# Optimization experiments

Hardware: AMD Instinct MI355X
Metric: run time of the kernel (lower is better)

The kernel has to match this reference:

```python
import jax, jax.numpy as jnp
import numpy as np

B, S, D, H = 4, 2048, 256, 4
DH = D // H
MAX_LEN = 2048


def setup_inputs() -> dict:
    key = jax.random.key(0)
    ks = jax.random.split(key, 12)
    std = 0.02
    inp = {
        "x": jax.random.normal(ks[0], (B, S, D), dtype=jnp.float32),
        "Wq": jax.random.normal(ks[1], (D, D), dtype=jnp.float32) * std,
        "bq": jnp.zeros((D,), dtype=jnp.float32),
        "Wk": jax.random.normal(ks[2], (D, D), dtype=jnp.float32) * std,
        "bk": jnp.zeros((D,), dtype=jnp.float32),
        "Wv": jax.random.normal(ks[3], (D, D), dtype=jnp.float32) * std,
        "bv": jnp.zeros((D,), dtype=jnp.float32),
        "Wo": jax.random.normal(ks[4], (D, D), dtype=jnp.float32) * std,
        "bo": jnp.zeros((D,), dtype=jnp.float32),
        "rel_bias": jax.random.normal(ks[5], (2 * MAX_LEN - 1, H), dtype=jnp.float32) * std,
        "scale": jnp.ones((1,), dtype=jnp.float32) * np.sqrt(DH).astype(np.float32),
        "mask": jnp.ones((B, S), dtype=jnp.int32),
    }
    return inp


def reference(x, Wq, bq, Wk, bk, Wv, bv, Wo, bo, rel_bias, scale, mask):
    b, s, d = x.shape
    # projections (torch Linear: x @ W.T + b), split heads -> (B, H, S, Dh)
    def proj(W, bias):
        return (x @ W.T + bias).reshape(b, s, H, DH).transpose(0, 2, 1, 3)
    Q, K, V = proj(Wq, bq), proj(Wk, bk), proj(Wv, bv)

    # raw (un-softmaxed) scores: (B, H, S, S)
    scores = jnp.einsum("bhqd,bhkd->bhqk", Q, K) / scale[0]

    # relative-position bias gather: idx[i,j] = j - i + s - 1
    seq = jnp.arange(s)
    rel_idx = seq[None, :] - seq[:, None] + s - 1        # (S, S)
    rbias = rel_bias[rel_idx]                            # (S, S, H)
    scores = scores + rbias.transpose(2, 0, 1)[None]     # (1, H, S, S)

    # pairwise padding mask: mask_ij = mask_i * mask_j
    m2 = (mask[:, None, :, None] * mask[:, None, None, :])  # (B, 1, S, S)
    scores = jnp.where(m2 == 0, -jnp.inf, scores)

    # no softmax: plain weighted sum with V
    out = jnp.einsum("bhqk,bhkd->bhqd", scores, V)
    out = out.transpose(0, 2, 1, 3).reshape(b, s, d)
    return out @ Wo.T + bo
```

## Files before the change

kernel.cpp:

```cpp
#include <hip/hip_runtime.h>

#define BB 4
#define SS 2048
#define DD 256
#define HH 4
#define DHH 64
#define NDT 63

typedef unsigned short u16;
typedef __attribute__((ext_vector_type(8))) short bf16x8;
typedef __attribute__((ext_vector_type(4))) float f32x4;

#define MFMA(a, b, c) __builtin_amdgcn_mfma_f32_16x16x32_bf16((a), (b), (c), 0, 0, 0)


__device__ __forceinline__ u16 f2b(float x) {
    union { float f; unsigned u; } v; v.f = x;
    unsigned r = (v.u + 0x7FFFu + ((v.u >> 16) & 1u)) >> 16;
    return (u16)r;
}

__global__ __launch_bounds__(256) void cast_x(
    const float* __restrict__ x, u16* __restrict__ Xkb)
{
    const int th = blockIdx.x * 256 + threadIdx.x;
    const int t = th >> 5;
    const int F0 = (th & 31) * 8;
    float4 a = *(const float4*)(x + (size_t)t * DD + F0);
    float4 b = *(const float4*)(x + (size_t)t * DD + F0 + 4);
    u16 v[8] = { f2b(a.x), f2b(a.y), f2b(a.z), f2b(a.w),
                 f2b(b.x), f2b(b.y), f2b(b.z), f2b(b.w) };
    *(uint4*)(Xkb + (size_t)(F0 >> 5) * 262144 + (size_t)t * 32 + (F0 & 31)) = *(uint4*)v;
}

__global__ __launch_bounds__(256) void cast_w(
    const float* __restrict__ Wq, const float* __restrict__ Wk,
    const float* __restrict__ Wv, const float* __restrict__ Wo,
    u16* __restrict__ Wkb)
{
    const float* src = (blockIdx.y == 0) ? Wq : (blockIdx.y == 1) ? Wk
                     : (blockIdx.y == 2) ? Wv : Wo;
    const int th = blockIdx.x * 256 + threadIdx.x;
    const int o = th >> 5;
    const int k0 = (th & 31) * 8;
    float4 a = *(const float4*)(src + (size_t)o * DD + k0);
    float4 b = *(const float4*)(src + (size_t)o * DD + k0 + 4);
    u16 v[8] = { f2b(a.x), f2b(a.y), f2b(a.z), f2b(a.w),
                 f2b(b.x), f2b(b.y), f2b(b.z), f2b(b.w) };
    *(uint4*)(Wkb + (size_t)blockIdx.y * 65536 + (size_t)(k0 >> 5) * 8192
              + (size_t)o * 32 + (k0 & 31)) = *(uint4*)v;
}

__global__ __launch_bounds__(256) void zero_M(float* __restrict__ Mt)
{
    const int i = blockIdx.x * 256 + threadIdx.x;
    if (i < BB * HH * DHH * DHH) Mt[i] = 0.f;
}

__global__ __launch_bounds__(256) void rtiles_kernel(
    const float* __restrict__ rel_bias, u16* __restrict__ Rtb)
{
    const int h  = blockIdx.x / NDT;
    const int dt = blockIdx.x % NDT;
    const int tid = threadIdx.x;
    const int qq = tid >> 2;
    const int kf0 = (tid & 3) * 16;
    const int base = (dt - 31) * 64 - qq + (SS - 1);

    u16 v[16];
    #pragma unroll
    for (int m = 0; m < 16; ++m)
        v[m] = f2b(rel_bias[(size_t)(base + kf0 + m) * HH + h]);

    u16* dst = Rtb + ((size_t)(h * NDT + dt) * 2 + (kf0 >> 5)) * 2048
             + qq * 32 + (kf0 & 31);
    *(uint4*)dst       = *(uint4*)&v[0];
    *(uint4*)(dst + 8) = *(uint4*)&v[8];
}

__global__ __launch_bounds__(256) void proj_mfma(
    const u16* __restrict__ Xkb, const u16* __restrict__ Wkb,
    const float* __restrict__ bq, const float* __restrict__ bk,
    const float* __restrict__ bv,
    u16* __restrict__ Qkb, u16* __restrict__ Kkb, u16* __restrict__ Vkb)
{
    const int z = blockIdx.z;
    const u16* W = Wkb + (size_t)z * 65536;
    const float* bias = (z == 0) ? bq : (z == 1) ? bk : bv;

    const int tid = threadIdx.x;
    const int w = tid >> 6;
    const int lane = tid & 63;
    const int l15 = lane & 15;
    const int g = lane >> 4;

    const int n0 = blockIdx.x * 64;
    const int o0 = blockIdx.y * 128;

    f32x4 acc[4][2] = {};

    if (z == 0) {
        const int tw = w & 1, ow = w >> 1;
        #pragma unroll
        for (int kb = 0; kb < 8; ++kb) {
            bf16x8 bfrag[2], afrag[4];
            #pragma unroll
            for (int j = 0; j < 2; ++j)
                bfrag[j] = *(const bf16x8*)(Xkb + (size_t)kb * 262144
                          + (size_t)(n0 + tw * 32 + j * 16 + l15) * 32 + g * 8);
            #pragma unroll
            for (int f = 0; f < 4; ++f)
                afrag[f] = *(const bf16x8*)(W + (size_t)kb * 8192
                          + (size_t)(o0 + ow * 64 + f * 16 + l15) * 32 + g * 8);
            #pragma unroll
            for (int f = 0; f < 4; ++f)
                #pragma unroll
                for (int j = 0; j < 2; ++j)
                    acc[f][j] = MFMA(afrag[f], bfrag[j], acc[f][j]);
        }
        #pragma unroll
        for (int f = 0; f < 4; ++f) {
            const int F = o0 + ow * 64 + f * 16 + g * 4;
            float4 bv4 = *(const float4*)(bias + F);
            #pragma unroll
            for (int j = 0; j < 2; ++j) {
                const int t = n0 + tw * 32 + j * 16 + l15;
                const int b = t >> 11, q = t & 2047;
                ushort4 st = { f2b(acc[f][j].x + bv4.x), f2b(acc[f][j].y + bv4.y),
                               f2b(acc[f][j].z + bv4.z), f2b(acc[f][j].w + bv4.w) };
                *(ushort4*)(Qkb + (size_t)b * 524288 + (size_t)(F >> 5) * 65536
                            + (size_t)q * 32 + (F & 31)) = st;
            }
        }
    } else {
        #pragma unroll
        for (int kb = 0; kb < 8; ++kb) {
            bf16x8 bfrag[2], afrag[4];
            #pragma unroll
            for (int j = 0; j < 2; ++j)
                bfrag[j] = *(const bf16x8*)(W + (size_t)kb * 8192
                          + (size_t)(o0 + w * 32 + j * 16 + l15) * 32 + g * 8);
            #pragma unroll
            for (int f = 0; f < 4; ++f)
                afrag[f] = *(const bf16x8*)(Xkb + (size_t)kb * 262144
                          + (size_t)(n0 + f * 16 + l15) * 32 + g * 8);
            #pragma unroll
            for (int f = 0; f < 4; ++f)
                #pragma unroll
                for (int j = 0; j < 2; ++j)
                    acc[f][j] = MFMA(afrag[f], bfrag[j], acc[f][j]);
        }
        u16* T = (z == 1) ? Kkb : Vkb;
        const int b = n0 >> 11;
        const int tloc = n0 & 2047;
        #pragma unroll
        for (int j = 0; j < 2; ++j) {
            const int o = o0 + w * 32 + j * 16 + l15;
            const int h = o >> 6, d = o & 63;
            const float bb = bias[o];
            u16* dst0 = T + (size_t)(b * HH + h) * 131072 + (size_t)d * 32;
            #pragma unroll
            for (int f = 0; f < 4; ++f) {
                const int kblk = (tloc >> 5) + (f >> 1);
                const int off = (f & 1) * 16 + g * 4;
                ushort4 st = { f2b(acc[f][j].x + bb), f2b(acc[f][j].y + bb),
                               f2b(acc[f][j].z + bb), f2b(acc[f][j].w + bb) };
                *(ushort4*)(dst0 + (size_t)kblk * 2048 + off) = st;
            }
        }
    }
}

__global__ __launch_bounds__(256) void calc_M_mfma(
    const u16* __restrict__ Kkb, const u16* __restrict__ Vkb,
    const float* __restrict__ scale, float* __restrict__ Mt)
{
    const int bh = blockIdx.x;
    const int kb0 = blockIdx.y * 8;

    const int tid = threadIdx.x;
    const int w = tid >> 6;
    const int lane = tid & 63;
    const int l15 = lane & 15;
    const int g = lane >> 4;

    const u16* Vb = Vkb + (size_t)bh * 131072;
    const u16* Kb = Kkb + (size_t)bh * 131072;

    f32x4 acc[4] = {};
    #pragma unroll
    for (int kk = 0; kk < 8; ++kk) {
        const size_t kb = kb0 + kk;
        bf16x8 bfrag = *(const bf16x8*)(Kb + kb * 2048 + (size_t)(w * 16 + l15) * 32 + g * 8);
        #pragma unroll
        for (int f = 0; f < 4; ++f) {
            bf16x8 afrag = *(const bf16x8*)(Vb + kb * 2048 + (size_t)(f * 16 + l15) * 32 + g * 8);
            acc[f] = MFMA(afrag, bfrag, acc[f]);
        }
    }

    const float inv_scale = 1.0f / scale[0];
    float* Mg = Mt + (size_t)bh * 4096;
    const int e = w * 16 + l15;
    #pragma unroll
    for (int f = 0; f < 4; ++f) {
        const float* a = (const float*)&acc[f];
        #pragma unroll
        for (int i = 0; i < 4; ++i)
            atomicAdd(Mg + (f * 16 + g * 4 + i) * DHH + e, a[i] * inv_scale);
    }
}

__global__ __launch_bounds__(256) void cvt_M(
    const float* __restrict__ Mt, u16* __restrict__ Mkb)
{
    const int bh = blockIdx.x;
    const int tid = threadIdx.x;
    const int d = tid >> 2;
    const int c = (tid & 3) * 16;
    const float* src = Mt + (size_t)bh * 4096 + d * 64 + c;
    u16 v[16];
    #pragma unroll
    for (int m = 0; m < 16; ++m) v[m] = f2b(src[m]);
    u16* dst = Mkb + (size_t)bh * 4096 + (size_t)(c >> 5) * 2048 + d * 32 + (c & 31);
    *(uint4*)dst       = *(uint4*)&v[0];
    *(uint4*)(dst + 8) = *(uint4*)&v[8];
}

__global__ __launch_bounds__(256) void attn_mfma(
    const u16* __restrict__ Qkb, const u16* __restrict__ Vkb,
    const u16* __restrict__ Mkb, const u16* __restrict__ Rtb,
    u16* __restrict__ attnkb)
{
    const int bh = blockIdx.x;
    const int b = bh >> 2, h = bh & 3;
    const int qs = blockIdx.y;

    const int tid = threadIdx.x;
    const int w = tid >> 6;
    const int lane = tid & 63;
    const int l15 = lane & 15;
    const int g = lane >> 4;

    const int qt = qs * 2 + (w >> 1);
    const int qq0 = (w & 1) * 32;

    const u16* vb = Vkb + (size_t)bh * 131072 + (size_t)l15 * 32 + g * 8;
    const u16* rb = Rtb + (size_t)h * NDT * 4096 + (size_t)(qq0 + l15) * 32 + g * 8;

    f32x4 acc[4][2] = {};
    bf16x8 A0[4], B0[2], A1[4], B1[2];

#define LOAD_IT(it_, A_, B_) do {                                           \
        const int it__ = (it_);                                             \
        const u16* vp = vb + (size_t)it__ * 2048;                           \
        _Pragma("unroll")                                                   \
        for (int f = 0; f < 4; ++f) A_[f] = *(const bf16x8*)(vp + f * 512); \
        const int dt__ = (it__ >> 1) - qt + 31;                             \
        const u16* rp = rb + (size_t)(dt__ * 2 + (it__ & 1)) * 2048;        \
        _Pragma("unroll")                                                   \
        for (int j = 0; j < 2; ++j) B_[j] = *(const bf16x8*)(rp + j * 512); \
    } while (0)

#define MFMA_IT(A_, B_) do {                                                \
        _Pragma("unroll")                                                   \
        for (int f = 0; f < 4; ++f)                                         \
            _Pragma("unroll")                                               \
            for (int j = 0; j < 2; ++j)                                     \
                acc[f][j] = MFMA(A_[f], B_[j], acc[f][j]);                  \
    } while (0)

    LOAD_IT(0, A0, B0);
    LOAD_IT(1, A1, B1);
    for (int it = 0; it < 64; it += 2) {
        MFMA_IT(A0, B0);
        LOAD_IT((it + 2) & 63, A0, B0);
        MFMA_IT(A1, B1);
        LOAD_IT((it + 3) & 63, A1, B1);
    }
#undef LOAD_IT
#undef MFMA_IT

    const int q0w = qs * 128 + w * 32;
    #pragma unroll
    for (int s2 = 0; s2 < 2; ++s2) {
        bf16x8 bfrag[2], afrag[4];
        #pragma unroll
        for (int j = 0; j < 2; ++j)
            bfrag[j] = *(const bf16x8*)(Qkb + (size_t)b * 524288
                      + (size_t)(h * 2 + s2) * 65536
                      + (size_t)(q0w + j * 16 + l15) * 32 + g * 8);
        #pragma unroll
        for (int f = 0; f < 4; ++f)
            afrag[f] = *(const bf16x8*)(Mkb + (size_t)bh * 4096 + (size_t)s2 * 2048
                      + (size_t)(f * 16 + l15) * 32 + g * 8);
        #pragma unroll
        for (int f = 0; f < 4; ++f)
            #pragma unroll
            for (int j = 0; j < 2; ++j)
                acc[f][j] = MFMA(afrag[f], bfrag[j], acc[f][j]);
    }

    #pragma unroll
    for (int f = 0; f < 4; ++f) {
        const int Fb = h * 2 + (f >> 1);
        const int off = (f & 1) * 16 + g * 4;
        #pragma unroll
        for (int j = 0; j < 2; ++j) {
            const int q = q0w + j * 16 + l15;
            ushort4 st = { f2b(acc[f][j].x), f2b(acc[f][j].y),
                           f2b(acc[f][j].z), f2b(acc[f][j].w) };
            *(ushort4*)(attnkb + (size_t)b * 524288 + (size_t)Fb * 65536
                        + (size_t)q * 32 + off) = st;
        }
    }
}

__global__ __launch_bounds__(256) void gemm_out_mfma(
    const u16* __restrict__ attnkb, const u16* __restrict__ Wokb,
    const float* __restrict__ bo, float* __restrict__ out)
{
    const int tid = threadIdx.x;
    const int w = tid >> 6;
    const int lane = tid & 63;
    const int l15 = lane & 15;
    const int g = lane >> 4;

    const int n0 = blockIdx.x * 64;
    const int o0 = blockIdx.y * 128;
    const int tw = w & 1, ow = w >> 1;

    f32x4 acc[4][2] = {};
    #pragma unroll
    for (int kb = 0; kb < 8; ++kb) {
        bf16x8 bfrag[2], afrag[4];
        #pragma unroll
        for (int j = 0; j < 2; ++j) {
            const int t = n0 + tw * 32 + j * 16 + l15;
            const int b = t >> 11, q = t & 2047;
            bfrag[j] = *(const bf16x8*)(attnkb + (size_t)b * 524288
                      + (size_t)kb * 65536 + (size_t)q * 32 + g * 8);
        }
        #pragma unroll
        for (int f = 0; f < 4; ++f)
            afrag[f] = *(const bf16x8*)(Wokb + (size_t)kb * 8192
                      + (size_t)(o0 + ow * 64 + f * 16 + l15) * 32 + g * 8);
        #pragma unroll
        for (int f = 0; f < 4; ++f)
            #pragma unroll
            for (int j = 0; j < 2; ++j)
                acc[f][j] = MFMA(afrag[f], bfrag[j], acc[f][j]);
    }

    #pragma unroll
    for (int f = 0; f < 4; ++f) {
        const int o = o0 + ow * 64 + f * 16 + g * 4;
        float4 bv4 = *(const float4*)(bo + o);
        #pragma unroll
        for (int j = 0; j < 2; ++j) {
            const int t = n0 + tw * 32 + j * 16 + l15;
            float4 st = { acc[f][j].x + bv4.x, acc[f][j].y + bv4.y,
                          acc[f][j].z + bv4.z, acc[f][j].w + bv4.w };
            *(float4*)(out + (size_t)t * DD + o) = st;
        }
    }
}

extern "C" void kernel_launch(void* const* d_in, const int* in_sizes, int n_in,
                              void* d_out, int out_size, void* d_ws, size_t ws_size,
                              hipStream_t stream)
{
    const float* x        = (const float*)d_in[0];
    const float* Wq       = (const float*)d_in[1];
    const float* bq       = (const float*)d_in[2];
    const float* Wk       = (const float*)d_in[3];
    const float* bk       = (const float*)d_in[4];
    const float* Wv       = (const float*)d_in[5];
    const float* bv       = (const float*)d_in[6];
    const float* Wo       = (const float*)d_in[7];
    const float* bo       = (const float*)d_in[8];
    const float* rel_bias = (const float*)d_in[9];
    const float* scale    = (const float*)d_in[10];

    float* out = (float*)d_out;

    const size_t NP = (size_t)BB * SS * DD;
    float* Mt    = (float*)d_ws;
    u16*   Xkb   = (u16*)(Mt + 65536);
    u16*   Wkb   = Xkb + NP;
    u16*   Qkb   = Wkb + 4 * 65536;
    u16*   Kkb   = Qkb + NP;
    u16*   Vkb   = Kkb + NP;
    u16*   attnk = Vkb + NP;
    u16*   Rtb   = attnk + NP;
    u16*   Mkb   = Rtb + (size_t)HH * NDT * 4096;

    cast_x<<<dim3(1024), dim3(256), 0, stream>>>(x, Xkb);
    cast_w<<<dim3(32, 4), dim3(256), 0, stream>>>(Wq, Wk, Wv, Wo, Wkb);
    zero_M<<<dim3(256), dim3(256), 0, stream>>>(Mt);
    rtiles_kernel<<<dim3(HH * NDT), dim3(256), 0, stream>>>(rel_bias, Rtb);

    proj_mfma<<<dim3(128, 2, 3), dim3(256), 0, stream>>>(
        Xkb, Wkb, bq, bk, bv, Qkb, Kkb, Vkb);

    calc_M_mfma<<<dim3(BB * HH, 8), dim3(256), 0, stream>>>(Kkb, Vkb, scale, Mt);
    cvt_M<<<dim3(BB * HH), dim3(256), 0, stream>>>(Mt, Mkb);

    attn_mfma<<<dim3(BB * HH, 16), dim3(256), 0, stream>>>(
        Qkb, Vkb, Mkb, Rtb, attnk);

    gemm_out_mfma<<<dim3(128, 2), dim3(256), 0, stream>>>(
        attnk, Wkb + 3 * 65536, bo, out);
}
```

Measured before the change: 144.6 us.

## Merge prep kernels, split attention over key halves, drop M atomics

Fuses the four preprocessing kernels into one launch. The atomic accumulation of M is replaced by per-split partial buffers, which the attention kernel sums and converts on the fly, so the zero and convert kernels go away. The attention kernel now gives each wave a 64-query tile and splits the key dimension into two halves across blockIdx.z, writing two partial outputs. The output GEMM then reads and sums both. This cuts launch count and atomics and improves MFMA reuse per fragment, at the cost of an extra intermediate buffer and doubled reads in the output GEMM.

```diff
diff --git a/kernel.cpp b/kernel.cpp
--- a/kernel.cpp
+++ b/kernel.cpp
@@ -20,62 +20,53 @@
     return (u16)r;
 }
 
-__global__ __launch_bounds__(256) void cast_x(
-    const float* __restrict__ x, u16* __restrict__ Xkb)
-{
-    const int th = blockIdx.x * 256 + threadIdx.x;
-    const int t = th >> 5;
-    const int F0 = (th & 31) * 8;
-    float4 a = *(const float4*)(x + (size_t)t * DD + F0);
-    float4 b = *(const float4*)(x + (size_t)t * DD + F0 + 4);
-    u16 v[8] = { f2b(a.x), f2b(a.y), f2b(a.z), f2b(a.w),
-                 f2b(b.x), f2b(b.y), f2b(b.z), f2b(b.w) };
-    *(uint4*)(Xkb + (size_t)(F0 >> 5) * 262144 + (size_t)t * 32 + (F0 & 31)) = *(uint4*)v;
-}
-
-__global__ __launch_bounds__(256) void cast_w(
+__global__ __launch_bounds__(256) void prep(
+    const float* __restrict__ x,
     const float* __restrict__ Wq, const float* __restrict__ Wk,
     const float* __restrict__ Wv, const float* __restrict__ Wo,
-    u16* __restrict__ Wkb)
-{
-    const float* src = (blockIdx.y == 0) ? Wq : (blockIdx.y == 1) ? Wk
-                     : (blockIdx.y == 2) ? Wv : Wo;
-    const int th = blockIdx.x * 256 + threadIdx.x;
-    const int o = th >> 5;
-    const int k0 = (th & 31) * 8;
-    float4 a = *(const float4*)(src + (size_t)o * DD + k0);
-    float4 b = *(const float4*)(src + (size_t)o * DD + k0 + 4);
-    u16 v[8] = { f2b(a.x), f2b(a.y), f2b(a.z), f2b(a.w),
-                 f2b(b.x), f2b(b.y), f2b(b.z), f2b(b.w) };
-    *(uint4*)(Wkb + (size_t)blockIdx.y * 65536 + (size_t)(k0 >> 5) * 8192
-              + (size_t)o * 32 + (k0 & 31)) = *(uint4*)v;
-}
-
-__global__ __launch_bounds__(256) void zero_M(float* __restrict__ Mt)
-{
-    const int i = blockIdx.x * 256 + threadIdx.x;
-    if (i < BB * HH * DHH * DHH) Mt[i] = 0.f;
-}
-
-__global__ __launch_bounds__(256) void rtiles_kernel(
-    const float* __restrict__ rel_bias, u16* __restrict__ Rtb)
-{
-    const int h  = blockIdx.x / NDT;
-    const int dt = blockIdx.x % NDT;
+    const float* __restrict__ rel_bias,
+    u16* __restrict__ Xkb, u16* __restrict__ Wkb, u16* __restrict__ Rtb)
+{
+    const int bx = blockIdx.x;
     const int tid = threadIdx.x;
-    const int qq = tid >> 2;
-    const int kf0 = (tid & 3) * 16;
-    const int base = (dt - 31) * 64 - qq + (SS - 1);
-
-    u16 v[16];
-    #pragma unroll
-    for (int m = 0; m < 16; ++m)
-        v[m] = f2b(rel_bias[(size_t)(base + kf0 + m) * HH + h]);
-
-    u16* dst = Rtb + ((size_t)(h * NDT + dt) * 2 + (kf0 >> 5)) * 2048
-             + qq * 32 + (kf0 & 31);
-    *(uint4*)dst       = *(uint4*)&v[0];
-    *(uint4*)(dst + 8) = *(uint4*)&v[8];
+
+    if (bx < 1024) {
+        const int th = bx * 256 + tid;
+        const int t = th >> 5;
+        const int F0 = (th & 31) * 8;
+        float4 a = *(const float4*)(x + (size_t)t * DD + F0);
+        float4 b = *(const float4*)(x + (size_t)t * DD + F0 + 4);
+        u16 v[8] = { f2b(a.x), f2b(a.y), f2b(a.z), f2b(a.w),
+                     f2b(b.x), f2b(b.y), f2b(b.z), f2b(b.w) };
+        *(uint4*)(Xkb + (size_t)(F0 >> 5) * 262144 + (size_t)t * 32 + (F0 & 31)) = *(uint4*)v;
+    } else if (bx < 1152) {
+        const int m = (bx - 1024) >> 5;
+        const float* src = (m == 0) ? Wq : (m == 1) ? Wk : (m == 2) ? Wv : Wo;
+        const int th = ((bx - 1024) & 31) * 256 + tid;
+        const int o = th >> 5;
+        const int k0 = (th & 31) * 8;
+        float4 a = *(const float4*)(src + (size_t)o * DD + k0);
+        float4 b = *(const float4*)(src + (size_t)o * DD + k0 + 4);
+        u16 v[8] = { f2b(a.x), f2b(a.y), f2b(a.z), f2b(a.w),
+                     f2b(b.x), f2b(b.y), f2b(b.z), f2b(b.w) };
+        *(uint4*)(Wkb + (size_t)m * 65536 + (size_t)(k0 >> 5) * 8192
+                  + (size_t)o * 32 + (k0 & 31)) = *(uint4*)v;
+    } else {
+        const int r = bx - 1152;
+        const int h  = r / NDT;
+        const int dt = r % NDT;
+        const int qq = tid >> 2;
+        const int kf0 = (tid & 3) * 16;
+        const int base = (dt - 31) * 64 - qq + (SS - 1);
+        u16 v[16];
+        #pragma unroll
+        for (int m2 = 0; m2 < 16; ++m2)
+            v[m2] = f2b(rel_bias[(size_t)(base + kf0 + m2) * HH + h]);
+        u16* dst = Rtb + ((size_t)(h * NDT + dt) * 2 + (kf0 >> 5)) * 2048
+                 + qq * 32 + (kf0 & 31);
+        *(uint4*)dst       = *(uint4*)&v[0];
+        *(uint4*)(dst + 8) = *(uint4*)&v[8];
+    }
 }
 
 __global__ __launch_bounds__(256) void proj_mfma(
@@ -173,10 +164,10 @@
 
 __global__ __launch_bounds__(256) void calc_M_mfma(
     const u16* __restrict__ Kkb, const u16* __restrict__ Vkb,
-    const float* __restrict__ scale, float* __restrict__ Mt)
+    const float* __restrict__ scale, float* __restrict__ Mt4)
 {
     const int bh = blockIdx.x;
-    const int kb0 = blockIdx.y * 8;
+    const int ks = blockIdx.y;
 
     const int tid = threadIdx.x;
     const int w = tid >> 6;
@@ -189,8 +180,8 @@
 
     f32x4 acc[4] = {};
     #pragma unroll
-    for (int kk = 0; kk < 8; ++kk) {
-        const size_t kb = kb0 + kk;
+    for (int kk = 0; kk < 16; ++kk) {
+        const size_t kb = ks * 16 + kk;
         bf16x8 bfrag = *(const bf16x8*)(Kb + kb * 2048 + (size_t)(w * 16 + l15) * 32 + g * 8);
         #pragma unroll
         for (int f = 0; f < 4; ++f) {
@@ -200,41 +191,26 @@
     }
 
     const float inv_scale = 1.0f / scale[0];
-    float* Mg = Mt + (size_t)bh * 4096;
+    float* Mg = Mt4 + ((size_t)ks * 16 + bh) * 4096;
     const int e = w * 16 + l15;
     #pragma unroll
     for (int f = 0; f < 4; ++f) {
         const float* a = (const float*)&acc[f];
         #pragma unroll
         for (int i = 0; i < 4; ++i)
-            atomicAdd(Mg + (f * 16 + g * 4 + i) * DHH + e, a[i] * inv_scale);
-    }
-}
-
-__global__ __launch_bounds__(256) void cvt_M(
-    const float* __restrict__ Mt, u16* __restrict__ Mkb)
-{
-    const int bh = blockIdx.x;
-    const int tid = threadIdx.x;
-    const int d = tid >> 2;
-    const int c = (tid & 3) * 16;
-    const float* src = Mt + (size_t)bh * 4096 + d * 64 + c;
-    u16 v[16];
-    #pragma unroll
-    for (int m = 0; m < 16; ++m) v[m] = f2b(src[m]);
-    u16* dst = Mkb + (size_t)bh * 4096 + (size_t)(c >> 5) * 2048 + d * 32 + (c & 31);
-    *(uint4*)dst       = *(uint4*)&v[0];
-    *(uint4*)(dst + 8) = *(uint4*)&v[8];
-}
-
-__global__ __launch_bounds__(256) void attn_mfma(
+            Mg[(f * 16 + g * 4 + i) * DHH + e] = a[i] * inv_scale;
+    }
+}
+
+__global__ __launch_bounds__(256, 1) void attn_mfma(
     const u16* __restrict__ Qkb, const u16* __restrict__ Vkb,
-    const u16* __restrict__ Mkb, const u16* __restrict__ Rtb,
-    u16* __restrict__ attnkb)
+    const float* __restrict__ Mt4, const u16* __restrict__ Rtb,
+    u16* __restrict__ attnA, u16* __restrict__ attnB)
 {
     const int bh = blockIdx.x;
     const int b = bh >> 2, h = bh & 3;
     const int qs = blockIdx.y;
+    const int ks = blockIdx.z;
 
     const int tid = threadIdx.x;
     const int w = tid >> 6;
@@ -242,82 +218,100 @@
     const int l15 = lane & 15;
     const int g = lane >> 4;
 
-    const int qt = qs * 2 + (w >> 1);
-    const int qq0 = (w & 1) * 32;
-
-    const u16* vb = Vkb + (size_t)bh * 131072 + (size_t)l15 * 32 + g * 8;
-    const u16* rb = Rtb + (size_t)h * NDT * 4096 + (size_t)(qq0 + l15) * 32 + g * 8;
-
-    f32x4 acc[4][2] = {};
-    bf16x8 A0[4], B0[2], A1[4], B1[2];
-
-#define LOAD_IT(it_, A_, B_) do {                                           \
-        const int it__ = (it_);                                             \
-        const u16* vp = vb + (size_t)it__ * 2048;                           \
-        _Pragma("unroll")                                                   \
-        for (int f = 0; f < 4; ++f) A_[f] = *(const bf16x8*)(vp + f * 512); \
-        const int dt__ = (it__ >> 1) - qt + 31;                             \
-        const u16* rp = rb + (size_t)(dt__ * 2 + (it__ & 1)) * 2048;        \
-        _Pragma("unroll")                                                   \
-        for (int j = 0; j < 2; ++j) B_[j] = *(const bf16x8*)(rp + j * 512); \
+    const int qt64 = qs * 4 + w;
+
+    const u16* vb = Vkb + (size_t)bh * 131072 + (size_t)l15 * 32 + g * 8
+                  + (size_t)ks * 32 * 2048;
+    const u16* rb = Rtb + (size_t)h * NDT * 4096 + (size_t)l15 * 32 + g * 8;
+
+    f32x4 acc[4][4] = {};
+    bf16x8 A0[4], B0[4], A1[4], B1[4];
+
+#define LOAD_IT(it_, A_, B_) do {                                            \
+        const int it__ = (it_) & 31;                                         \
+        const u16* vp = vb + (size_t)it__ * 2048;                            \
+        _Pragma("unroll")                                                    \
+        for (int f = 0; f < 4; ++f) A_[f] = *(const bf16x8*)(vp + f * 512);  \
+        const int dt__ = ((ks * 32 + it__) >> 1) - qt64 + 31;                \
+        const u16* rp = rb + (size_t)(dt__ * 2 + (it__ & 1)) * 2048;         \
+        _Pragma("unroll")                                                    \
+        for (int j = 0; j < 4; ++j) B_[j] = *(const bf16x8*)(rp + j * 512);  \
     } while (0)
 
-#define MFMA_IT(A_, B_) do {                                                \
-        _Pragma("unroll")                                                   \
-        for (int f = 0; f < 4; ++f)                                         \
-            _Pragma("unroll")                                               \
-            for (int j = 0; j < 2; ++j)                                     \
-                acc[f][j] = MFMA(A_[f], B_[j], acc[f][j]);                  \
+#define MFMA_IT(A_, B_) do {                                                 \
+        _Pragma("unroll")                                                    \
+        for (int f = 0; f < 4; ++f)                                          \
+            _Pragma("unroll")                                                \
+            for (int j = 0; j < 4; ++j)                                      \
+                acc[f][j] = MFMA(A_[f], B_[j], acc[f][j]);                   \
     } while (0)
 
     LOAD_IT(0, A0, B0);
     LOAD_IT(1, A1, B1);
-    for (int it = 0; it < 64; it += 2) {
+    for (int it = 0; it < 32; it += 2) {
         MFMA_IT(A0, B0);
-        LOAD_IT((it + 2) & 63, A0, B0);
+        LOAD_IT(it + 2, A0, B0);
         MFMA_IT(A1, B1);
-        LOAD_IT((it + 3) & 63, A1, B1);
+        LOAD_IT(it + 3, A1, B1);
     }
 #undef LOAD_IT
 #undef MFMA_IT
 
-    const int q0w = qs * 128 + w * 32;
-    #pragma unroll
-    for (int s2 = 0; s2 < 2; ++s2) {
-        bf16x8 bfrag[2], afrag[4];
-        #pragma unroll
-        for (int j = 0; j < 2; ++j)
-            bfrag[j] = *(const bf16x8*)(Qkb + (size_t)b * 524288
-                      + (size_t)(h * 2 + s2) * 65536
-                      + (size_t)(q0w + j * 16 + l15) * 32 + g * 8);
-        #pragma unroll
-        for (int f = 0; f < 4; ++f)
-            afrag[f] = *(const bf16x8*)(Mkb + (size_t)bh * 4096 + (size_t)s2 * 2048
-                      + (size_t)(f * 16 + l15) * 32 + g * 8);
-        #pragma unroll
-        for (int f = 0; f < 4; ++f)
-            #pragma unroll
-            for (int j = 0; j < 2; ++j)
-                acc[f][j] = MFMA(afrag[f], bfrag[j], acc[f][j]);
-    }
-
+    const int qbase = qt64 * 64;
+
+    if (ks == 0) {
+        #pragma unroll
+        for (int s2 = 0; s2 < 2; ++s2) {
+            bf16x8 bfrag[4], afrag[4];
+            #pragma unroll
+            for (int j = 0; j < 4; ++j)
+                bfrag[j] = *(const bf16x8*)(Qkb + (size_t)b * 524288
+                          + (size_t)(h * 2 + s2) * 65536
+                          + (size_t)(qbase + j * 16 + l15) * 32 + g * 8);
+            #pragma unroll
+            for (int f = 0; f < 4; ++f) {
+                const float* mp = Mt4 + (size_t)bh * 4096
+                                + (size_t)(f * 16 + l15) * DHH + s2 * 32 + g * 8;
+                float m8[8] = {};
+                #pragma unroll
+                for (int p = 0; p < 4; ++p) {
+                    float4 a = *(const float4*)(mp + (size_t)p * 65536);
+                    float4 c = *(const float4*)(mp + (size_t)p * 65536 + 4);
+                    m8[0] += a.x; m8[1] += a.y; m8[2] += a.z; m8[3] += a.w;
+                    m8[4] += c.x; m8[5] += c.y; m8[6] += c.z; m8[7] += c.w;
+                }
+                u16 t8[8];
+                #pragma unroll
+                for (int e = 0; e < 8; ++e) t8[e] = f2b(m8[e]);
+                afrag[f] = *(bf16x8*)t8;
+            }
+            #pragma unroll
+            for (int f = 0; f < 4; ++f)
+                #pragma unroll
+                for (int j = 0; j < 4; ++j)
+                    acc[f][j] = MFMA(afrag[f], bfrag[j], acc[f][j]);
+        }
+    }
+
+    u16* dstbuf = (ks == 0) ? attnA : attnB;
     #pragma unroll
     for (int f = 0; f < 4; ++f) {
         const int Fb = h * 2 + (f >> 1);
         const int off = (f & 1) * 16 + g * 4;
         #pragma unroll
-        for (int j = 0; j < 2; ++j) {
-            const int q = q0w + j * 16 + l15;
+        for (int j = 0; j < 4; ++j) {
+            const int q = qbase + j * 16 + l15;
             ushort4 st = { f2b(acc[f][j].x), f2b(acc[f][j].y),
                            f2b(acc[f][j].z), f2b(acc[f][j].w) };
-            *(ushort4*)(attnkb + (size_t)b * 524288 + (size_t)Fb * 65536
+            *(ushort4*)(dstbuf + (size_t)b * 524288 + (size_t)Fb * 65536
                         + (size_t)q * 32 + off) = st;
         }
     }
 }
 
 __global__ __launch_bounds__(256) void gemm_out_mfma(
-    const u16* __restrict__ attnkb, const u16* __restrict__ Wokb,
+    const u16* __restrict__ attnA, const u16* __restrict__ attnB,
+    const u16* __restrict__ Wokb,
     const float* __restrict__ bo, float* __restrict__ out)
 {
     const int tid = threadIdx.x;
@@ -333,13 +327,15 @@
     f32x4 acc[4][2] = {};
     #pragma unroll
     for (int kb = 0; kb < 8; ++kb) {
-        bf16x8 bfrag[2], afrag[4];
+        bf16x8 bfA[2], bfB[2], afrag[4];
         #pragma unroll
         for (int j = 0; j < 2; ++j) {
             const int t = n0 + tw * 32 + j * 16 + l15;
             const int b = t >> 11, q = t & 2047;
-            bfrag[j] = *(const bf16x8*)(attnkb + (size_t)b * 524288
-                      + (size_t)kb * 65536 + (size_t)q * 32 + g * 8);
+            const size_t base = (size_t)b * 524288 + (size_t)kb * 65536
+                              + (size_t)q * 32 + g * 8;
+            bfA[j] = *(const bf16x8*)(attnA + base);
+            bfB[j] = *(const bf16x8*)(attnB + base);
         }
         #pragma unroll
         for (int f = 0; f < 4; ++f)
@@ -348,8 +344,10 @@
         #pragma unroll
         for (int f = 0; f < 4; ++f)
             #pragma unroll
-            for (int j = 0; j < 2; ++j)
-                acc[f][j] = MFMA(afrag[f], bfrag[j], acc[f][j]);
+            for (int j = 0; j < 2; ++j) {
+                acc[f][j] = MFMA(afrag[f], bfA[j], acc[f][j]);
+                acc[f][j] = MFMA(afrag[f], bfB[j], acc[f][j]);
+            }
     }
 
     #pragma unroll
@@ -385,30 +383,27 @@
     float* out = (float*)d_out;
 
     const size_t NP = (size_t)BB * SS * DD;
-    float* Mt    = (float*)d_ws;
-    u16*   Xkb   = (u16*)(Mt + 65536);
+    float* Mt4   = (float*)d_ws;
+    u16*   Xkb   = (u16*)(Mt4 + 262144);
     u16*   Wkb   = Xkb + NP;
     u16*   Qkb   = Wkb + 4 * 65536;
     u16*   Kkb   = Qkb + NP;
     u16*   Vkb   = Kkb + NP;
-    u16*   attnk = Vkb + NP;
-    u16*   Rtb   = attnk + NP;
-    u16*   Mkb   = Rtb + (size_t)HH * NDT * 4096;
-
-    cast_x<<<dim3(1024), dim3(256), 0, stream>>>(x, Xkb);
-    cast_w<<<dim3(32, 4), dim3(256), 0, stream>>>(Wq, Wk, Wv, Wo, Wkb);
-    zero_M<<<dim3(256), dim3(256), 0, stream>>>(Mt);
-    rtiles_kernel<<<dim3(HH * NDT), dim3(256), 0, stream>>>(rel_bias, Rtb);
+    u16*   attnA = Vkb + NP;
+    u16*   attnB = attnA + NP;
+    u16*   Rtb   = attnB + NP;
+
+    prep<<<dim3(1404), dim3(256), 0, stream>>>(
+        x, Wq, Wk, Wv, Wo, rel_bias, Xkb, Wkb, Rtb);
 
     proj_mfma<<<dim3(128, 2, 3), dim3(256), 0, stream>>>(
         Xkb, Wkb, bq, bk, bv, Qkb, Kkb, Vkb);
 
-    calc_M_mfma<<<dim3(BB * HH, 8), dim3(256), 0, stream>>>(Kkb, Vkb, scale, Mt);
-    cvt_M<<<dim3(BB * HH), dim3(256), 0, stream>>>(Mt, Mkb);
-
-    attn_mfma<<<dim3(BB * HH, 16), dim3(256), 0, stream>>>(
-        Qkb, Vkb, Mkb, Rtb, attnk);
+    calc_M_mfma<<<dim3(BB * HH, 4), dim3(256), 0, stream>>>(Kkb, Vkb, scale, Mt4);
+
+    attn_mfma<<<dim3(BB * HH, 8, 2), dim3(256), 0, stream>>>(
+        Qkb, Vkb, Mt4, Rtb, attnA, attnB);
 
     gemm_out_mfma<<<dim3(128, 2), dim3(256), 0, stream>>>(
-        attnk, Wkb + 3 * 65536, bo, out);
-}
+        attnA, attnB, Wkb + 3 * 65536, bo, out);
+}
```

After: 136.6 us. -5.5%, faster.
